# Kernel tuning notes

Measured on AMD Instinct MI355X. Metric: run time of the kernel, lower is better.

The kernel has to match this reference:

```python
import jax, jax.numpy as jnp
import numpy as np
from jax import lax

B, T, D, U = 128, 1024, 256, 64


def setup_inputs() -> dict:
    key = jax.random.key(0)
    ks = jax.random.split(key, 6)
    x = jax.random.normal(ks[0], (B, T, D), jnp.float32)
    W = jax.random.normal(ks[1], (D, U), jnp.float32) / np.sqrt(D).astype(np.float32)
    b = jnp.zeros((U,), jnp.float32)
    # chain kernel (transition matrix); tfa uses Orthogonal init, a scaled normal is fine as a stand-in
    trans = jax.random.normal(ks[2], (U, U), jnp.float32) * 0.1
    left = jnp.zeros((U,), jnp.float32)   # boundary_initializer=Zeros
    right = jnp.zeros((U,), jnp.float32)
    tags = jax.random.randint(ks[3], (B, T), 0, U, dtype=jnp.int32)
    lengths = jax.random.randint(ks[4], (B,), T // 2, T + 1, dtype=jnp.int32)
    return dict(x=x, W=W, b=b, trans=trans, left=left, right=right, tags=tags, lengths=lengths)


def _potentials(x, W, b, left, right, lengths):
    pot = jnp.einsum('btd,du->btu', x, W) + b                      # [B,T,U] unary potentials
    t_idx = jnp.arange(T)
    is_first = (t_idx == 0)[None, :, None]                          # boundary energies (use_boundary=True)
    is_last = (t_idx[None, :] == (lengths - 1)[:, None])[:, :, None]
    pot = pot + jnp.where(is_first, left, 0.0) + jnp.where(is_last, right, 0.0)
    return pot


def reference(x, W, b, trans, left, right, tags, lengths):
    pot = _potentials(x, W, b, left, right, lengths)                # [B,T,U]
    valid = jnp.arange(T)[None, :] < lengths[:, None]               # [B,T]

    pot_rest = jnp.swapaxes(pot[:, 1:], 0, 1)                       # [T-1,B,U]
    valid_rest = valid[:, 1:].T                                     # [T-1,B]

    # ---- log partition (forward algorithm, masked logsumexp scan) ----
    def fwd_step(alpha, inp):
        pot_t, v_t = inp
        new = jax.nn.logsumexp(alpha[:, :, None] + trans[None], axis=1) + pot_t
        return jnp.where(v_t[:, None], new, alpha), None

    alpha, _ = lax.scan(fwd_step, pot[:, 0], (pot_rest, valid_rest))
    log_norm = jax.nn.logsumexp(alpha, axis=1)                      # [B]

    # ---- gold sequence score ----
    unary = jnp.sum(jnp.take_along_axis(pot, tags[:, :, None], axis=2)[:, :, 0]
                    * valid.astype(pot.dtype), axis=1)
    binary = jnp.sum(trans[tags[:, :-1], tags[:, 1:]] * valid[:, 1:].astype(pot.dtype), axis=1)
    loss = -jnp.mean(unary + binary - log_norm)                     # -crf_log_likelihood, reduced

    # ---- Viterbi decode (max-product scan + backtrack) ----
    ident = jnp.arange(U, dtype=jnp.int32)[None, :]

    def vit_step(alpha, inp):
        pot_t, v_t = inp
        scores = alpha[:, :, None] + trans[None]                    # [B,U,U]
        bp = jnp.argmax(scores, axis=1).astype(jnp.int32)           # [B,U]
        new = jnp.max(scores, axis=1) + pot_t
        bp = jnp.where(v_t[:, None], bp, ident)                     # identity bp past seq end
        return jnp.where(v_t[:, None], new, alpha), bp

    valpha, bps = lax.scan(vit_step, pot[:, 0], (pot_rest, valid_rest))  # bps: [T-1,B,U]
    last_tag = jnp.argmax(valpha, axis=1).astype(jnp.int32)         # [B]

    def back_step(tag, bp):
        prev = jnp.take_along_axis(bp, tag[:, None], axis=1)[:, 0]
        return prev, prev

    _, rev_tags = lax.scan(back_step, last_tag, bps, reverse=True)  # [T-1,B]
    decode = jnp.swapaxes(jnp.concatenate([rev_tags, last_tag[None]], axis=0), 0, 1)  # [B,T]
    decode = jnp.where(valid, decode, 0)

    return loss, decode, pot
```

## Files before the change

kernel.cpp:

```cpp
#include <hip/hip_runtime.h>

#define BB 128
#define TT 1024
#define DD 256
#define UU 64

#define WAVE_LDS_FENCE() asm volatile("s_waitcnt lgkmcnt(0)" ::: "memory")

__global__ __launch_bounds__(256) void pot_kernel(
    const float* __restrict__ x, const float* __restrict__ W,
    const float* __restrict__ bvec, const float* __restrict__ left,
    const float* __restrict__ right, const int* __restrict__ lengths,
    float* __restrict__ pot)
{
  const int tid = threadIdx.x;
  const int lane = tid & 63;
  const int w = tid >> 6;
  const int rowblk = (int)blockIdx.x * 64;
  const int wloc = __builtin_amdgcn_readfirstlane(w * 16);
  const int rbase = rowblk + wloc;

  __shared__ __align__(16) float xs[2][64][64];

  const float* gsrc = x + (size_t)(rowblk + wloc + (lane >> 4)) * DD + (lane & 15) * 4;

#define STAGE_KT(ktv, bufv)                                                   \
  {                                                                           \
    _Pragma("unroll")                                                         \
    for (int q = 0; q < 4; ++q) {                                             \
      const float* gp = gsrc + (size_t)q * 4 * DD + (ktv) * 64;               \
      float* lp = &xs[(bufv)][wloc + q * 4][0];                               \
      __builtin_amdgcn_global_load_lds(                                       \
          (const __attribute__((address_space(1))) void*)gp,                  \
          (__attribute__((address_space(3))) void*)lp, 16, 0, 0);             \
    }                                                                         \
  }

  STAGE_KT(0, 0)
  __syncthreads();

  float acc[16];
#pragma unroll
  for (int i = 0; i < 16; ++i) acc[i] = 0.f;

#pragma unroll 1
  for (int kt = 0; kt < 4; ++kt) {
    const int buf = kt & 1;
    if (kt < 3) STAGE_KT(kt + 1, buf ^ 1)

    float wreg[64];
#pragma unroll
    for (int j = 0; j < 64; ++j)
      wreg[j] = W[(size_t)(kt * 64 + j) * UU + lane];

#pragma unroll
    for (int i = 0; i < 16; ++i) {
      const float4* xr4 = (const float4*)&xs[buf][wloc + i][0];
#pragma unroll
      for (int jv = 0; jv < 16; ++jv) {
        float4 xv = xr4[jv];
        acc[i] = fmaf(xv.x, wreg[jv * 4 + 0], acc[i]);
        acc[i] = fmaf(xv.y, wreg[jv * 4 + 1], acc[i]);
        acc[i] = fmaf(xv.z, wreg[jv * 4 + 2], acc[i]);
        acc[i] = fmaf(xv.w, wreg[jv * 4 + 3], acc[i]);
      }
    }

    __syncthreads();
  }
#undef STAGE_KT

  const float bb = bvec[lane];
  const float lf = left[lane];
  const float rg = right[lane];
#pragma unroll
  for (int i = 0; i < 16; ++i) {
    int r = rbase + i;
    int bidx = r >> 10;
    int t = r & (TT - 1);
    int len = lengths[bidx];
    float v = acc[i] + bb;
    if (t == 0) v += lf;
    if (t == len - 1) v += rg;
    pot[(size_t)r * UU + lane] = v;
  }
}

__global__ __launch_bounds__(64)
__attribute__((amdgpu_waves_per_eu(1, 1))) void scan_kernel(
    const float* __restrict__ pot, const float* __restrict__ trans,
    const int* __restrict__ lengths,
    unsigned char* __restrict__ bp, float* __restrict__ log_norm,
    int* __restrict__ last_tag, float* __restrict__ valpha, int fast)
{
  const int lane = threadIdx.x;
  const int b = blockIdx.x & (BB - 1);
  const bool is_vit = blockIdx.x >= BB;
  const int len = lengths[b];
  const float* potb = pot + (size_t)b * TT * UU;

  __shared__ __align__(16) float sh[2][64];

#define RLF(au, v) __uint_as_float(__builtin_amdgcn_readlane((au), (v)))

  if (!is_vit) {
    float tE[64];
#pragma unroll
    for (int v = 0; v < 64; ++v)
      tE[v] = __expf(trans[v * UU + lane]);

    float A = __expf(potb[lane]);
    int C = 0;

    float pe1 = __expf(potb[UU + lane]);
    float pe2 = __expf(potb[2 * UU + lane]);
    float pe3 = __expf(potb[3 * UU + lane]);
    float pr4 = potb[4 * UU + lane];
    float pr5 = potb[5 * UU + lane];
    float pr6 = potb[6 * UU + lane];
    float pr7 = potb[7 * UU + lane];

#pragma unroll 1
    for (int t = 1; t < len; ++t) {
      float pcur = pe1;
      pe1 = pe2; pe2 = pe3;
      pe3 = __expf(pr4);
      pr4 = pr5; pr5 = pr6; pr6 = pr7;
      int tp = t + 7 < TT ? t + 7 : TT - 1;
      pr7 = potb[(size_t)tp * UU + lane];

      const unsigned Au = __float_as_uint(A);
      float s0 = 0.f, s1 = 0.f, s2 = 0.f, s3 = 0.f;
#pragma unroll
      for (int vg = 0; vg < 4; ++vg) {
        float bc[16];
#pragma unroll
        for (int c = 0; c < 16; ++c)
          bc[c] = RLF(Au, vg * 16 + c);
        __builtin_amdgcn_sched_barrier(0);
#pragma unroll
        for (int c = 0; c < 4; ++c) {
          s0 = fmaf(bc[c],      tE[vg * 16 + 0 + c],  s0);
          s1 = fmaf(bc[4 + c],  tE[vg * 16 + 4 + c],  s1);
          s2 = fmaf(bc[8 + c],  tE[vg * 16 + 8 + c],  s2);
          s3 = fmaf(bc[12 + c], tE[vg * 16 + 12 + c], s3);
        }
      }
      float sum = (s0 + s1) + (s2 + s3);
      A = sum * pcur;
      if ((t & 3) == 0) {
        unsigned ab = __builtin_amdgcn_readfirstlane(__float_as_uint(A));
        int k = (int)((ab >> 23) & 0xffu) - 127;
        C += k;
        A = __builtin_ldexpf(A, -k);
      }
    }
    float e = A;
#pragma unroll
    for (int off = 32; off > 0; off >>= 1)
      e += __shfl_xor(e, off);
    if (lane == 0) log_norm[b] = __logf(e) + (float)C * 0.69314718056f;
  } else {
    float tT[64];
#pragma unroll
    for (int v = 0; v < 64; ++v)
      tT[v] = trans[v * UU + lane];

    float va = potb[lane];

    if (fast) {
      float* vab = valpha + (size_t)b * TT * UU;
      vab[lane] = va;
      float pn1 = potb[UU + lane];
      float pn2 = potb[2 * UU + lane];
      float pn3 = potb[3 * UU + lane];
      float pn4 = potb[4 * UU + lane];

#pragma unroll 1
      for (int t = 1; t < len; ++t) {
        float pcur = pn1;
        pn1 = pn2; pn2 = pn3; pn3 = pn4;
        int tp = t + 4 < TT ? t + 4 : TT - 1;
        pn4 = potb[(size_t)tp * UU + lane];

        const unsigned Vu = __float_as_uint(va);
        float m0 = -3.4e38f, m1 = -3.4e38f, m2 = -3.4e38f, m3 = -3.4e38f;
#pragma unroll
        for (int vg = 0; vg < 4; ++vg) {
          float bc[16];
#pragma unroll
          for (int c = 0; c < 16; ++c)
            bc[c] = RLF(Vu, vg * 16 + c);
          __builtin_amdgcn_sched_barrier(0);
          m0 = fmaxf(fmaxf(fmaxf(fmaxf(
                   bc[0] + tT[vg * 16 + 0],
                   bc[1] + tT[vg * 16 + 1]),
                   bc[2] + tT[vg * 16 + 2]),
                   bc[3] + tT[vg * 16 + 3]), m0);
          m1 = fmaxf(fmaxf(fmaxf(fmaxf(
                   bc[4] + tT[vg * 16 + 4],
                   bc[5] + tT[vg * 16 + 5]),
                   bc[6] + tT[vg * 16 + 6]),
                   bc[7] + tT[vg * 16 + 7]), m1);
          m2 = fmaxf(fmaxf(fmaxf(fmaxf(
                   bc[8] + tT[vg * 16 + 8],
                   bc[9] + tT[vg * 16 + 9]),
                   bc[10] + tT[vg * 16 + 10]),
                   bc[11] + tT[vg * 16 + 11]), m2);
          m3 = fmaxf(fmaxf(fmaxf(fmaxf(
                   bc[12] + tT[vg * 16 + 12],
                   bc[13] + tT[vg * 16 + 13]),
                   bc[14] + tT[vg * 16 + 14]),
                   bc[15] + tT[vg * 16 + 15]), m3);
        }
        float m = fmaxf(fmaxf(m0, m1), fmaxf(m2, m3));
        va = m + pcur;
        vab[(size_t)t * UU + lane] = va;
      }
    } else {
      float pn1 = potb[UU + lane];
      float pn2 = potb[2 * UU + lane];
      float pn3 = potb[3 * UU + lane];
      unsigned char* bpb = bp + (size_t)b * TT * UU;

#pragma unroll 1
      for (int t = 1; t < len; ++t) {
        const int p = t & 1;
        sh[p][lane] = va;
        float pcur = pn1;
        pn1 = pn2; pn2 = pn3;
        int tp = t + 3 < TT ? t + 3 : TT - 1;
        pn3 = potb[(size_t)tp * UU + lane];
        WAVE_LDS_FENCE();
        const float4* sh4 = (const float4*)sh[p];
        float mc[8];
        int ac[8];
#pragma unroll
        for (int c = 0; c < 8; ++c) {
          float m = -3.4e38f;
          int am = 0;
#pragma unroll
          for (int q = 0; q < 2; ++q) {
            float4 a4 = sh4[c * 2 + q];
            int base = c * 8 + q * 4;
            float s;
            s = a4.x + tT[base + 0]; if (s > m) { m = s; am = base + 0; }
            s = a4.y + tT[base + 1]; if (s > m) { m = s; am = base + 1; }
            s = a4.z + tT[base + 2]; if (s > m) { m = s; am = base + 2; }
            s = a4.w + tT[base + 3]; if (s > m) { m = s; am = base + 3; }
          }
          mc[c] = m; ac[c] = am;
        }
        float m = mc[0]; int am = ac[0];
#pragma unroll
        for (int c = 1; c < 8; ++c) {
          if (mc[c] > m) { m = mc[c]; am = ac[c]; }
        }
        va = m + pcur;
        bpb[(size_t)(t - 1) * UU + lane] = (unsigned char)am;
      }

      {
        const int off = lane * 4;
        const unsigned b0 = (unsigned)(off & 63);
        const unsigned pattern = b0 | ((b0 + 1) << 8) | ((b0 + 2) << 16) | ((b0 + 3) << 24);
#pragma unroll 1
        for (int r0 = len - 1; r0 < TT - 1; r0 += 4) {
          int row = r0 + (off >> 6);
          if (row < TT - 1)
            *(unsigned*)(bpb + (size_t)row * UU + (off & 63)) = pattern;
        }
      }
    }

    float v = va;
    int idx = lane;
#pragma unroll
    for (int off = 32; off > 0; off >>= 1) {
      float vo = __shfl_down(v, off);
      int io = __shfl_down(idx, off);
      if (vo > v || (vo == v && io < idx)) { v = vo; idx = io; }
    }
    if (lane == 0) last_tag[b] = idx;
  }
#undef RLF
}

__global__ __launch_bounds__(256) void bp_kernel(
    const float* __restrict__ valpha, const float* __restrict__ trans,
    const int* __restrict__ lengths, unsigned char* __restrict__ bp)
{
  const int lane = threadIdx.x & 63;
  const int w = __builtin_amdgcn_readfirstlane((int)(threadIdx.x >> 6));
  const int b = blockIdx.x >> 6;
  const int rg = ((int)(blockIdx.x & 63)) * 16 + w * 4;
  const int len = lengths[b];

  float tcol[64];
#pragma unroll
  for (int v = 0; v < 64; ++v)
    tcol[v] = trans[v * UU + lane];

  unsigned char* bpb = bp + (size_t)b * TT * UU;
#pragma unroll
  for (int k = 0; k < 4; ++k) {
    int r = rg + k;
    if (r >= TT - 1) continue;
    if (r >= len - 1) {
      bpb[(size_t)r * UU + lane] = (unsigned char)lane;
    } else {
      const float* vr = valpha + ((size_t)b * TT + r) * UU;
      float m = vr[0] + tcol[0];
      int am = 0;
#pragma unroll
      for (int v = 1; v < 64; ++v) {
        float s = vr[v] + tcol[v];
        if (s > m) { m = s; am = v; }
      }
      bpb[(size_t)r * UU + lane] = (unsigned char)am;
    }
  }
}

__global__ __launch_bounds__(64)
__attribute__((amdgpu_waves_per_eu(1, 1))) void decode_kernel(
    const float* __restrict__ pot, const float* __restrict__ trans,
    const int* __restrict__ tags, const int* __restrict__ lengths,
    const unsigned char* __restrict__ bp, const float* __restrict__ log_norm,
    const int* __restrict__ last_tag, float* __restrict__ score,
    float* __restrict__ dec_out)
{
  const int lane = threadIdx.x;
  const int b = blockIdx.x;
  const int len = lengths[b];
  const float* potb = pot + (size_t)b * TT * UU;
  const int* tagb = tags + (size_t)b * TT;

  float s = 0.f;
#pragma unroll 1
  for (int i = 0; i < TT / 64; ++i) {
    int t = i * 64 + lane;
    if (t < len) {
      int tg = tagb[t];
      s += potb[(size_t)t * UU + tg];
      if (t > 0) s += trans[tagb[t - 1] * UU + tg];
    }
  }
#pragma unroll
  for (int off = 32; off > 0; off >>= 1)
    s += __shfl_xor(s, off);
  if (lane == 0) score[b] = s - log_norm[b];

  __shared__ int sd[TT];
  const unsigned char* bpb = bp + (size_t)b * TT * UU;
  int tag = last_tag[b];
  if (lane == 0) sd[TT - 1] = tag;
#pragma unroll 1
  for (int tg = TT - 2; tg >= 0; tg -= 8) {
    unsigned char rows[8];
#pragma unroll
    for (int k = 0; k < 8; ++k) {
      int t = tg - k;
      rows[k] = (t >= 0) ? bpb[(size_t)t * UU + lane] : (unsigned char)0;
    }
#pragma unroll
    for (int k = 0; k < 8; ++k) {
      int t = tg - k;
      if (t >= 0) {
        int prev = __shfl((int)rows[k], tag);
        if (lane == 0) sd[t] = prev;
        tag = prev;
      }
    }
  }
  __syncthreads();
  float* db = dec_out + (size_t)b * TT;
#pragma unroll 1
  for (int i = 0; i < TT / 64; ++i) {
    int t = i * 64 + lane;
    db[t] = (t < len) ? (float)sd[t] : 0.f;
  }
}

__global__ __launch_bounds__(128) void loss_kernel(
    const float* __restrict__ score, float* __restrict__ out)
{
  int tid = threadIdx.x;
  float s = score[tid];
#pragma unroll
  for (int off = 32; off > 0; off >>= 1)
    s += __shfl_xor(s, off);
  __shared__ float partial[2];
  if ((tid & 63) == 0) partial[tid >> 6] = s;
  __syncthreads();
  if (tid == 0) out[0] = -(partial[0] + partial[1]) / (float)BB;
}

extern "C" void kernel_launch(void* const* d_in, const int* in_sizes, int n_in,
                              void* d_out, int out_size, void* d_ws, size_t ws_size,
                              hipStream_t stream)
{
  (void)in_sizes; (void)n_in; (void)out_size;
  const float* x      = (const float*)d_in[0];
  const float* W      = (const float*)d_in[1];
  const float* bvec   = (const float*)d_in[2];
  const float* trans  = (const float*)d_in[3];
  const float* left   = (const float*)d_in[4];
  const float* right  = (const float*)d_in[5];
  const int* tags     = (const int*)d_in[6];
  const int* lengths  = (const int*)d_in[7];

  float* out      = (float*)d_out;
  float* dec_out  = out + 1;
  float* pot      = out + 1 + (size_t)BB * TT;

  const size_t bpB = (size_t)BB * TT * UU;
  const size_t vaB = (size_t)BB * TT * UU * 4;
  const int fast = (ws_size >= bpB + vaB + 4096) ? 1 : 0;

  unsigned char* bp = (unsigned char*)d_ws;
  float* valpha     = (float*)((char*)d_ws + bpB);
  char* tail        = (char*)d_ws + bpB + (fast ? vaB : 0);
  float* log_norm   = (float*)tail;
  int*   last_tag   = (int*)(log_norm + BB);
  float* score      = (float*)(last_tag + BB);

  pot_kernel<<<(BB * TT) / 64, 256, 0, stream>>>(x, W, bvec, left, right, lengths, pot);
  scan_kernel<<<2 * BB, 64, 0, stream>>>(pot, trans, lengths, bp, log_norm, last_tag, valpha, fast);
  if (fast)
    bp_kernel<<<BB * 64, 256, 0, stream>>>(valpha, trans, lengths, bp);
  decode_kernel<<<BB, 64, 0, stream>>>(pot, trans, tags, lengths, bp, log_norm, last_tag, score, dec_out);
  loss_kernel<<<1, 128, 0, stream>>>(score, out);
}
```

Before: 828.2 us.

## Restructure potential GEMM to row-per-lane with uniform W loads and swizzled LDS

The projection kernel now uses one 64-lane wave per block, with each lane owning one output row and accumulating all 64 units in registers. W rows are read with wave-uniform addresses, which can become scalar loads, and x tiles are staged into an XOR-swizzled LDS layout to avoid bank conflicts. The double buffering is removed, so each tile load is waited on before compute. The backpointer kernel now loads the valpha row once per lane and broadcasts it with readlane instead of issuing 64 uniform global loads per row.

```diff
diff --git a/kernel.cpp b/kernel.cpp
--- a/kernel.cpp
+++ b/kernel.cpp
@@ -7,82 +7,77 @@
 
 #define WAVE_LDS_FENCE() asm volatile("s_waitcnt lgkmcnt(0)" ::: "memory")
 
-__global__ __launch_bounds__(256) void pot_kernel(
+__global__ __launch_bounds__(64) void pot_kernel(
     const float* __restrict__ x, const float* __restrict__ W,
     const float* __restrict__ bvec, const float* __restrict__ left,
     const float* __restrict__ right, const int* __restrict__ lengths,
     float* __restrict__ pot)
 {
-  const int tid = threadIdx.x;
-  const int lane = tid & 63;
-  const int w = tid >> 6;
+  const int lane = threadIdx.x;
   const int rowblk = (int)blockIdx.x * 64;
-  const int wloc = __builtin_amdgcn_readfirstlane(w * 16);
-  const int rbase = rowblk + wloc;
-
-  __shared__ __align__(16) float xs[2][64][64];
-
-  const float* gsrc = x + (size_t)(rowblk + wloc + (lane >> 4)) * DD + (lane & 15) * 4;
-
-#define STAGE_KT(ktv, bufv)                                                   \
-  {                                                                           \
-    _Pragma("unroll")                                                         \
-    for (int q = 0; q < 4; ++q) {                                             \
-      const float* gp = gsrc + (size_t)q * 4 * DD + (ktv) * 64;               \
-      float* lp = &xs[(bufv)][wloc + q * 4][0];                               \
-      __builtin_amdgcn_global_load_lds(                                       \
-          (const __attribute__((address_space(1))) void*)gp,                  \
-          (__attribute__((address_space(3))) void*)lp, 16, 0, 0);             \
-    }                                                                         \
-  }
-
-  STAGE_KT(0, 0)
-  __syncthreads();
-
-  float acc[16];
-#pragma unroll
-  for (int i = 0; i < 16; ++i) acc[i] = 0.f;
+  const int row = rowblk + lane;
+
+  __shared__ __align__(16) float xs[64][64];
+
+  const int sr4 = lane >> 4;
+  const int scl = lane & 15;
+
+  float acc[64];
+#pragma unroll
+  for (int u = 0; u < 64; ++u) acc[u] = 0.f;
 
 #pragma unroll 1
   for (int kt = 0; kt < 4; ++kt) {
-    const int buf = kt & 1;
-    if (kt < 3) STAGE_KT(kt + 1, buf ^ 1)
-
-    float wreg[64];
-#pragma unroll
-    for (int j = 0; j < 64; ++j)
-      wreg[j] = W[(size_t)(kt * 64 + j) * UU + lane];
-
-#pragma unroll
-    for (int i = 0; i < 16; ++i) {
-      const float4* xr4 = (const float4*)&xs[buf][wloc + i][0];
-#pragma unroll
-      for (int jv = 0; jv < 16; ++jv) {
-        float4 xv = xr4[jv];
-        acc[i] = fmaf(xv.x, wreg[jv * 4 + 0], acc[i]);
-        acc[i] = fmaf(xv.y, wreg[jv * 4 + 1], acc[i]);
-        acc[i] = fmaf(xv.z, wreg[jv * 4 + 2], acc[i]);
-        acc[i] = fmaf(xv.w, wreg[jv * 4 + 3], acc[i]);
-      }
-    }
-
-    __syncthreads();
-  }
-#undef STAGE_KT
-
-  const float bb = bvec[lane];
-  const float lf = left[lane];
-  const float rg = right[lane];
-#pragma unroll
-  for (int i = 0; i < 16; ++i) {
-    int r = rbase + i;
-    int bidx = r >> 10;
-    int t = r & (TT - 1);
-    int len = lengths[bidx];
-    float v = acc[i] + bb;
-    if (t == 0) v += lf;
-    if (t == len - 1) v += rg;
-    pot[(size_t)r * UU + lane] = v;
+#pragma unroll
+    for (int q = 0; q < 16; ++q) {
+      const int r = q * 4 + sr4;
+      const int cG = scl ^ (r & 15);
+      const float* gp = x + (size_t)(rowblk + r) * DD + kt * 64 + cG * 4;
+      float* lp = &xs[q * 4][0];
+      __builtin_amdgcn_global_load_lds(
+          (const __attribute__((address_space(1))) void*)gp,
+          (__attribute__((address_space(3))) void*)lp, 16, 0, 0);
+    }
+    asm volatile("s_waitcnt vmcnt(0)" ::: "memory");
+    __builtin_amdgcn_sched_barrier(0);
+
+#pragma unroll 1
+    for (int j = 0; j < 16; ++j) {
+      const float4 xv =
+          *(const float4*)&xs[lane][(j ^ scl) * 4];
+      const float* wr0 = W + (size_t)(kt * 64 + j * 4) * UU;
+#pragma unroll
+      for (int k = 0; k < 4; ++k) {
+        const float xd = (k == 0) ? xv.x : (k == 1) ? xv.y : (k == 2) ? xv.z : xv.w;
+        const float* wr = wr0 + k * UU;
+#pragma unroll
+        for (int u = 0; u < 64; ++u)
+          acc[u] = fmaf(xd, wr[u], acc[u]);
+      }
+    }
+    WAVE_LDS_FENCE();
+  }
+
+  const int bidx = row >> 10;
+  const int t = row & (TT - 1);
+  const int len = lengths[bidx];
+  const bool isf = (t == 0);
+  const bool isl = (t == len - 1);
+  float* pr = pot + (size_t)row * UU;
+#pragma unroll
+  for (int c = 0; c < 16; ++c) {
+    float4 v4;
+    float vv[4];
+#pragma unroll
+    for (int k = 0; k < 4; ++k) {
+      const int u = c * 4 + k;
+      float v = acc[u] + bvec[u];
+      if (isf) v += left[u];
+      if (isl) v += right[u];
+      vv[k] = v;
+    }
+    v4.x = vv[0]; v4.y = vv[1]; v4.z = vv[2]; v4.w = vv[3];
+    *(float4*)(pr + c * 4) = v4;
   }
 }
 
@@ -296,6 +291,8 @@
   const int rg = ((int)(blockIdx.x & 63)) * 16 + w * 4;
   const int len = lengths[b];
 
+#define RLF(au, v) __uint_as_float(__builtin_amdgcn_readlane((au), (v)))
+
   float tcol[64];
 #pragma unroll
   for (int v = 0; v < 64; ++v)
@@ -310,16 +307,18 @@
       bpb[(size_t)r * UU + lane] = (unsigned char)lane;
     } else {
       const float* vr = valpha + ((size_t)b * TT + r) * UU;
-      float m = vr[0] + tcol[0];
+      const unsigned avu = __float_as_uint(vr[lane]);
+      float m = RLF(avu, 0) + tcol[0];
       int am = 0;
 #pragma unroll
       for (int v = 1; v < 64; ++v) {
-        float s = vr[v] + tcol[v];
+        float s = RLF(avu, v) + tcol[v];
         if (s > m) { m = s; am = v; }
       }
       bpb[(size_t)r * UU + lane] = (unsigned char)am;
     }
   }
+#undef RLF
 }
 
 __global__ __launch_bounds__(64)
@@ -425,7 +424,7 @@
   int*   last_tag   = (int*)(log_norm + BB);
   float* score      = (float*)(last_tag + BB);
 
-  pot_kernel<<<(BB * TT) / 64, 256, 0, stream>>>(x, W, bvec, left, right, lengths, pot);
+  pot_kernel<<<(BB * TT) / 64, 64, 0, stream>>>(x, W, bvec, left, right, lengths, pot);
   scan_kernel<<<2 * BB, 64, 0, stream>>>(pot, trans, lengths, bp, log_norm, last_tag, valpha, fast);
   if (fast)
     bp_kernel<<<BB * 64, 256, 0, stream>>>(valpha, trans, lengths, bp);
```

New measurement: 836.7 us. About the same (+1.0%).

## Broadcast x and valpha via readlane instead of LDS staging and uniform loads

Applied to the files above, without the earlier changes.

The potentials GEMM no longer stages x tiles through LDS with async global-to-LDS copies. Each lane now loads one column of 16 rows, and values are broadcast across the wave with readlane while W rows are prefetched four at a time. The backpointer kernel likewise loads the valpha row once per lane and broadcasts it with readlane instead of issuing 64 uniform loads. This removes LDS traffic and barriers, but each readlane is a scalar instruction feeding an FMA, which may throttle VALU throughput.

```diff
diff --git a/kernel.cpp b/kernel.cpp
--- a/kernel.cpp
+++ b/kernel.cpp
@@ -13,31 +13,11 @@
     const float* __restrict__ right, const int* __restrict__ lengths,
     float* __restrict__ pot)
 {
-  const int tid = threadIdx.x;
-  const int lane = tid & 63;
-  const int w = tid >> 6;
-  const int rowblk = (int)blockIdx.x * 64;
-  const int wloc = __builtin_amdgcn_readfirstlane(w * 16);
-  const int rbase = rowblk + wloc;
-
-  __shared__ __align__(16) float xs[2][64][64];
-
-  const float* gsrc = x + (size_t)(rowblk + wloc + (lane >> 4)) * DD + (lane & 15) * 4;
-
-#define STAGE_KT(ktv, bufv)                                                   \
-  {                                                                           \
-    _Pragma("unroll")                                                         \
-    for (int q = 0; q < 4; ++q) {                                             \
-      const float* gp = gsrc + (size_t)q * 4 * DD + (ktv) * 64;               \
-      float* lp = &xs[(bufv)][wloc + q * 4][0];                               \
-      __builtin_amdgcn_global_load_lds(                                       \
-          (const __attribute__((address_space(1))) void*)gp,                  \
-          (__attribute__((address_space(3))) void*)lp, 16, 0, 0);             \
-    }                                                                         \
-  }
-
-  STAGE_KT(0, 0)
-  __syncthreads();
+  const int lane = threadIdx.x & 63;
+  const int w = threadIdx.x >> 6;
+  const int rbase = (int)blockIdx.x * 64 + w * 16;
+
+#define RLX(fv, l) __uint_as_float(__builtin_amdgcn_readlane(__float_as_uint(fv), (l)))
 
   float acc[16];
 #pragma unroll
@@ -45,30 +25,39 @@
 
 #pragma unroll 1
   for (int kt = 0; kt < 4; ++kt) {
-    const int buf = kt & 1;
-    if (kt < 3) STAGE_KT(kt + 1, buf ^ 1)
-
-    float wreg[64];
-#pragma unroll
-    for (int j = 0; j < 64; ++j)
-      wreg[j] = W[(size_t)(kt * 64 + j) * UU + lane];
-
-#pragma unroll
-    for (int i = 0; i < 16; ++i) {
-      const float4* xr4 = (const float4*)&xs[buf][wloc + i][0];
-#pragma unroll
-      for (int jv = 0; jv < 16; ++jv) {
-        float4 xv = xr4[jv];
-        acc[i] = fmaf(xv.x, wreg[jv * 4 + 0], acc[i]);
-        acc[i] = fmaf(xv.y, wreg[jv * 4 + 1], acc[i]);
-        acc[i] = fmaf(xv.z, wreg[jv * 4 + 2], acc[i]);
-        acc[i] = fmaf(xv.w, wreg[jv * 4 + 3], acc[i]);
-      }
-    }
-
-    __syncthreads();
-  }
-#undef STAGE_KT
+    float xr[16];
+#pragma unroll
+    for (int i = 0; i < 16; ++i)
+      xr[i] = x[(size_t)(rbase + i) * DD + kt * 64 + lane];
+
+    const float* Wk = W + (size_t)kt * 64 * UU;
+    float wc0 = Wk[0 * UU + lane];
+    float wc1 = Wk[1 * UU + lane];
+    float wc2 = Wk[2 * UU + lane];
+    float wc3 = Wk[3 * UU + lane];
+
+#pragma unroll 1
+    for (int jc = 0; jc < 16; ++jc) {
+      float wn0 = 0.f, wn1 = 0.f, wn2 = 0.f, wn3 = 0.f;
+      if (jc < 15) {
+        const float* Wn = Wk + (size_t)(jc * 4 + 4) * UU;
+        wn0 = Wn[0 * UU + lane];
+        wn1 = Wn[1 * UU + lane];
+        wn2 = Wn[2 * UU + lane];
+        wn3 = Wn[3 * UU + lane];
+      }
+      const int jb = jc * 4;
+#pragma unroll
+      for (int i = 0; i < 16; ++i) {
+        acc[i] = fmaf(RLX(xr[i], jb + 0), wc0, acc[i]);
+        acc[i] = fmaf(RLX(xr[i], jb + 1), wc1, acc[i]);
+        acc[i] = fmaf(RLX(xr[i], jb + 2), wc2, acc[i]);
+        acc[i] = fmaf(RLX(xr[i], jb + 3), wc3, acc[i]);
+      }
+      wc0 = wn0; wc1 = wn1; wc2 = wn2; wc3 = wn3;
+    }
+  }
+#undef RLX
 
   const float bb = bvec[lane];
   const float lf = left[lane];
@@ -296,6 +285,8 @@
   const int rg = ((int)(blockIdx.x & 63)) * 16 + w * 4;
   const int len = lengths[b];
 
+#define RLF(au, v) __uint_as_float(__builtin_amdgcn_readlane((au), (v)))
+
   float tcol[64];
 #pragma unroll
   for (int v = 0; v < 64; ++v)
@@ -310,16 +301,18 @@
       bpb[(size_t)r * UU + lane] = (unsigned char)lane;
     } else {
       const float* vr = valpha + ((size_t)b * TT + r) * UU;
-      float m = vr[0] + tcol[0];
+      const unsigned avu = __float_as_uint(vr[lane]);
+      float m = RLF(avu, 0) + tcol[0];
       int am = 0;
 #pragma unroll
       for (int v = 1; v < 64; ++v) {
-        float s = vr[v] + tcol[v];
+        float s = RLF(avu, v) + tcol[v];
         if (s > m) { m = s; am = v; }
       }
       bpb[(size_t)r * UU + lane] = (unsigned char)am;
     }
   }
+#undef RLF
 }
 
 __global__ __launch_bounds__(64)
```

New measurement: 841.8 us. About the same (+1.7%).
